# Kernel tuning notes

Measured on AMD Instinct MI355X. Metric: run time of the kernel, lower is better.

## Reference

```python
import jax, jax.numpy as jnp
import numpy as np

B, S, D, E, H, K = 4, 4096, 256, 8, 512, 2  # batch, seq, d_model, n_experts, ffn_hidden(=2*D), top_k


def setup_inputs() -> dict:
    key = jax.random.key(0)
    ks = jax.random.split(key, 6)
    x = jax.random.normal(ks[0], (B, S, D), jnp.float32)
    Wg = jax.random.normal(ks[1], (D, E), jnp.float32) * 0.02
    bg = jnp.zeros((E,), jnp.float32)
    W1 = jax.random.normal(ks[2], (E, D, H), jnp.float32) * 0.02
    b1 = jnp.zeros((E, H), jnp.float32)
    W2 = jax.random.normal(ks[3], (E, H, D), jnp.float32) * 0.02
    b2 = jnp.zeros((E, D), jnp.float32)
    return {"x": x, "Wg": Wg, "bg": bg, "W1": W1, "b1": b1, "W2": W2, "b2": b2}


def reference(x, Wg, bg, W1, b1, W2, b2):
    Bv, Sv, Dv = x.shape
    # Gate: linear -> top_k indices. NOTE: the original computes softmax(top_k scores)
    # but never uses the probabilities in the combine, so only indices matter.
    gate_scores = x @ Wg + bg                      # [B,S,E]
    _, idx = jax.lax.top_k(gate_scores, K)          # [B,S,K] (distinct experts per token)
    # Boolean membership mask per expert (0/1), matching (expert_indices == i).any(-1)
    mask = jax.nn.one_hot(idx, E, dtype=x.dtype).sum(axis=-2)  # [B,S,E]

    xf = x.reshape(-1, Dv)                          # [T,D]
    mf = mask.reshape(-1, E)                        # [T,E]
    # Dense all-experts FFN, masked combine (faithful to unweighted scatter-add).
    h = jax.nn.gelu(jnp.einsum('td,edh->teh', xf, W1) + b1[None], approximate=False)  # [T,E,H]
    y = jnp.einsum('teh,ehd->ted', h, W2) + b2[None]                                   # [T,E,D]
    out = jnp.einsum('ted,te->td', y, mf)                                              # [T,D]
    return out.reshape(Bv, Sv, Dv)
```

## Files before the change

kernel.cpp:

```cpp
#include <hip/hip_runtime.h>
#include <hip/hip_bf16.h>

#define T_TOK 16384
#define DM 256
#define NE 8
#define HF 512
#define TM 32
#define XS_LD 264

typedef __bf16 bf16x8 __attribute__((ext_vector_type(8)));
typedef float f32x4 __attribute__((ext_vector_type(4)));
typedef unsigned short u16x8 __attribute__((ext_vector_type(8)));

#define MFMA16(a, b, c) __builtin_amdgcn_mfma_f32_16x16x32_bf16((a), (b), (c), 0, 0, 0)

__device__ __forceinline__ unsigned short f2bf(float f) {
  unsigned u = __float_as_uint(f);
  u += 0x7fffu + ((u >> 16) & 1u);
  return (unsigned short)(u >> 16);
}

__device__ __forceinline__ float gelu_f(float v) {
  float s = fabsf(v) * 0.70710678118654752f;
  float t = __builtin_amdgcn_rcpf(1.0f + 0.3275911f * s);
  float p = t * (0.254829592f +
            t * (-0.284496736f +
            t * (1.421413741f +
            t * (-1.453152027f + t * 1.061405429f))));
  float e = 1.0f - p * __expf(-s * s);
  e = copysignf(e, v);
  return 0.5f * v * (1.0f + e);
}

__device__ __forceinline__ void pack_body(const float* __restrict__ in,
                                          unsigned short* __restrict__ out,
                                          int K, int N, int idx) {
  int n = idx & (N - 1);
  int rest = idx / N;
  int kq = rest & ((K >> 3) - 1);
  int eidx = rest / (K >> 3);
  int k0 = kq * 8;
  const float* src = in + ((size_t)eidx * K + k0) * N + n;
  u16x8 pk;
#pragma unroll
  for (int j = 0; j < 8; j++) pk[j] = f2bf(src[(size_t)j * N]);
  size_t baseo = (size_t)eidx * K * N +
                 (size_t)((n >> 4) * (K >> 5) + (k0 >> 5)) * 512 +
                 (size_t)(((k0 >> 3) & 3) * 128 + (n & 15) * 8);
  *reinterpret_cast<u16x8*>(out + baseo) = pk;
}

__global__ __launch_bounds__(256) void prep_kernel(
    const float* __restrict__ W1, const float* __restrict__ W2,
    unsigned short* __restrict__ w1p, unsigned short* __restrict__ w2p,
    const float* __restrict__ x, unsigned short* __restrict__ x16,
    const float* __restrict__ Wg, const float* __restrict__ bg,
    int* __restrict__ cnts, int* __restrict__ list, float* __restrict__ out) {
  __shared__ float wg_s[DM * NE];
  __shared__ int hist[NE], base_s[NE], rank[NE];
  int b = blockIdx.x;
  int tid = threadIdx.x;
  if (b < 1024) {
    float4 z = make_float4(0.f, 0.f, 0.f, 0.f);
    float4* o4 = reinterpret_cast<float4*>(out) + ((size_t)b * 256 + tid) * 4;
#pragma unroll
    for (int j = 0; j < 4; j++) o4[j] = z;
    if (b < 512) pack_body(W1, w1p, DM, HF, b * 256 + tid);
    else         pack_body(W2, w2p, HF, DM, (b - 512) * 256 + tid);
    return;
  }
  int gb = b - 1024;
  {
    float4 wv0 = *reinterpret_cast<const float4*>(Wg + tid * 8);
    float4 wv1 = *reinterpret_cast<const float4*>(Wg + tid * 8 + 4);
    *reinterpret_cast<float4*>(&wg_s[tid * 8]) = wv0;
    *reinterpret_cast<float4*>(&wg_s[tid * 8 + 4]) = wv1;
  }
  if (tid < NE) { hist[tid] = 0; rank[tid] = 0; }
  __syncthreads();

  int tl = tid >> 2;
  int cg = tid & 3;
  int t = gb * 64 + tl;
  const float* xr = x + (size_t)t * DM + cg * 64;
  unsigned short* x16r = x16 + (size_t)t * DM + cg * 64;
  double acc[NE];
#pragma unroll
  for (int i = 0; i < NE; i++) acc[i] = 0.0;
  for (int d = 0; d < 64; d += 4) {
    float4 xv = *reinterpret_cast<const float4*>(xr + d);
    {
      unsigned long long pk = (unsigned long long)f2bf(xv.x) |
                              ((unsigned long long)f2bf(xv.y) << 16) |
                              ((unsigned long long)f2bf(xv.z) << 32) |
                              ((unsigned long long)f2bf(xv.w) << 48);
      *reinterpret_cast<unsigned long long*>(x16r + d) = pk;
    }
    const float* w0 = &wg_s[(cg * 64 + d) * NE];
    float xa[4] = {xv.x, xv.y, xv.z, xv.w};
#pragma unroll
    for (int dd = 0; dd < 4; dd++) {
      float4 wa = *reinterpret_cast<const float4*>(w0 + dd * NE);
      float4 wb = *reinterpret_cast<const float4*>(w0 + dd * NE + 4);
      double xd = (double)xa[dd];
      acc[0] += xd * (double)wa.x; acc[1] += xd * (double)wa.y;
      acc[2] += xd * (double)wa.z; acc[3] += xd * (double)wa.w;
      acc[4] += xd * (double)wb.x; acc[5] += xd * (double)wb.y;
      acc[6] += xd * (double)wb.z; acc[7] += xd * (double)wb.w;
    }
  }
#pragma unroll
  for (int i = 0; i < NE; i++) {
    acc[i] += __shfl_xor(acc[i], 1, 64);
    acc[i] += __shfl_xor(acc[i], 2, 64);
    acc[i] += (double)bg[i];
  }
  int e1 = 0;
#pragma unroll
  for (int i = 1; i < NE; i++) if (acc[i] > acc[e1]) e1 = i;
  int e2 = -1;
#pragma unroll
  for (int i = 0; i < NE; i++) {
    if (i == e1) continue;
    if (e2 < 0 || acc[i] > acc[e2]) e2 = i;
  }
  if (cg == 0) {
    atomicAdd(&hist[e1], 1);
    atomicAdd(&hist[e2], 1);
  }
  __syncthreads();
  if (tid < NE) base_s[tid] = atomicAdd(&cnts[tid], hist[tid]);
  __syncthreads();
  if (cg == 0) {
    int r1 = atomicAdd(&rank[e1], 1);
    list[e1 * T_TOK + base_s[e1] + r1] = t;
    int r2 = atomicAdd(&rank[e2], 1);
    list[e2 * T_TOK + base_s[e2] + r2] = t;
  }
}

__global__ __launch_bounds__(256, 4) void ffn_kernel(
    const unsigned short* __restrict__ x16, const unsigned short* __restrict__ w1p,
    const float* __restrict__ b1, const unsigned short* __restrict__ w2p,
    const float* __restrict__ b2, const int* __restrict__ cnts,
    const int* __restrict__ list, float* __restrict__ out) {
  __shared__ unsigned short Xs[TM * XS_LD];
  __shared__ unsigned short Hl[TM * XS_LD];
  __shared__ int tok[TM];

  int e = blockIdx.x & 7;
  int tile = blockIdx.x >> 3;
  int cnt = cnts[e];
  int base = tile * TM;
  if (base >= cnt) return;
  int rowsv = min(TM, cnt - base);

  int tid = threadIdx.x;
  int w = tid >> 6, lane = tid & 63;
  int quad = lane >> 4, l16 = lane & 15;

  const unsigned short* w1e = w1p + (size_t)e * (HF * DM) + lane * 8;
  const unsigned short* w2e = w2p + (size_t)e * (DM * HF) + lane * 8;

  bf16x8 bcur[4];
#pragma unroll
  for (int nt = 0; nt < 4; nt++)
    bcur[nt] = *reinterpret_cast<const bf16x8*>(w1e + (size_t)((w * 4 + nt) * 8) * 512);

  {
    int r = tid >> 3, cg = tid & 7;
    int token = -1;
    if (r < rowsv) token = list[e * T_TOK + base + r];
    if (cg == 0) tok[r] = token;
    unsigned short* xrow = &Xs[r * XS_LD + cg * 32];
    if (token >= 0) {
      const u16x8* src = reinterpret_cast<const u16x8*>(x16 + (size_t)token * DM + cg * 32);
#pragma unroll
      for (int j = 0; j < 4; j++)
        *reinterpret_cast<u16x8*>(xrow + j * 8) = src[j];
    } else {
      u16x8 z = {0, 0, 0, 0, 0, 0, 0, 0};
#pragma unroll
      for (int j = 0; j < 4; j++)
        *reinterpret_cast<u16x8*>(xrow + j * 8) = z;
    }
  }
  __syncthreads();

  f32x4 zero4 = {0.f, 0.f, 0.f, 0.f};
  f32x4 pacc[2][4];

#pragma unroll
  for (int mt = 0; mt < 2; mt++)
#pragma unroll
    for (int nt = 0; nt < 4; nt++) pacc[mt][nt] = zero4;
#pragma unroll
  for (int ks = 0; ks < 8; ks++) {
    bf16x8 bn[4];
#pragma unroll
    for (int nt = 0; nt < 4; nt++) {
      int tn = (ks < 7) ? (w * 4 + nt) : (16 + w * 4 + nt);
      int kk = (ks < 7) ? (ks + 1) : 0;
      bn[nt] = *reinterpret_cast<const bf16x8*>(w1e + (size_t)(tn * 8 + kk) * 512);
    }
    bf16x8 a[2];
#pragma unroll
    for (int mt = 0; mt < 2; mt++)
      a[mt] = *reinterpret_cast<const bf16x8*>(&Xs[(mt * 16 + l16) * XS_LD + ks * 32 + quad * 8]);
#pragma unroll
    for (int nt = 0; nt < 4; nt++)
#pragma unroll
      for (int mt = 0; mt < 2; mt++)
        pacc[mt][nt] = MFMA16(a[mt], bcur[nt], pacc[mt][nt]);
#pragma unroll
    for (int nt = 0; nt < 4; nt++) bcur[nt] = bn[nt];
  }
#pragma unroll
  for (int nt = 0; nt < 4; nt++) {
    float bias1 = b1[e * HF + w * 64 + nt * 16 + l16];
#pragma unroll
    for (int mt = 0; mt < 2; mt++)
#pragma unroll
      for (int r = 0; r < 4; r++) {
        int row = mt * 16 + quad * 4 + r;
        Hl[row * XS_LD + w * 64 + nt * 16 + l16] = f2bf(gelu_f(pacc[mt][nt][r] + bias1));
      }
  }

#pragma unroll
  for (int mt = 0; mt < 2; mt++)
#pragma unroll
    for (int nt = 0; nt < 4; nt++) pacc[mt][nt] = zero4;
#pragma unroll
  for (int ks = 0; ks < 8; ks++) {
    bf16x8 bn[4];
#pragma unroll
    for (int nt = 0; nt < 4; nt++) {
      if (ks < 7) {
        bn[nt] = *reinterpret_cast<const bf16x8*>(
            w1e + (size_t)((16 + w * 4 + nt) * 8 + ks + 1) * 512);
      } else {
        bn[nt] = *reinterpret_cast<const bf16x8*>(w2e + (size_t)((w * 4 + nt) * 16) * 512);
      }
    }
    bf16x8 a[2];
#pragma unroll
    for (int mt = 0; mt < 2; mt++)
      a[mt] = *reinterpret_cast<const bf16x8*>(&Xs[(mt * 16 + l16) * XS_LD + ks * 32 + quad * 8]);
#pragma unroll
    for (int nt = 0; nt < 4; nt++)
#pragma unroll
      for (int mt = 0; mt < 2; mt++)
        pacc[mt][nt] = MFMA16(a[mt], bcur[nt], pacc[mt][nt]);
#pragma unroll
    for (int nt = 0; nt < 4; nt++) bcur[nt] = bn[nt];
  }
  __syncthreads();
#pragma unroll
  for (int nt = 0; nt < 4; nt++) {
    float bias1 = b1[e * HF + 256 + w * 64 + nt * 16 + l16];
#pragma unroll
    for (int mt = 0; mt < 2; mt++)
#pragma unroll
      for (int r = 0; r < 4; r++) {
        int row = mt * 16 + quad * 4 + r;
        Xs[row * XS_LD + w * 64 + nt * 16 + l16] = f2bf(gelu_f(pacc[mt][nt][r] + bias1));
      }
  }
  __syncthreads();

  f32x4 oacc[2][4];
#pragma unroll
  for (int mt = 0; mt < 2; mt++)
#pragma unroll
    for (int nt = 0; nt < 4; nt++) oacc[mt][nt] = zero4;
#pragma unroll
  for (int ks2 = 0; ks2 < 16; ks2++) {
    bf16x8 bn[4];
    if (ks2 < 15) {
#pragma unroll
      for (int nt = 0; nt < 4; nt++)
        bn[nt] = *reinterpret_cast<const bf16x8*>(
            w2e + (size_t)((w * 4 + nt) * 16 + ks2 + 1) * 512);
    }
    const unsigned short* hbase = (ks2 < 8) ? Hl : Xs;
    int col = (ks2 & 7) * 32 + quad * 8;
    bf16x8 a[2];
#pragma unroll
    for (int mt = 0; mt < 2; mt++)
      a[mt] = *reinterpret_cast<const bf16x8*>(&hbase[(mt * 16 + l16) * XS_LD + col]);
#pragma unroll
    for (int nt = 0; nt < 4; nt++)
#pragma unroll
      for (int mt = 0; mt < 2; mt++)
        oacc[mt][nt] = MFMA16(a[mt], bcur[nt], oacc[mt][nt]);
    if (ks2 < 15) {
#pragma unroll
      for (int nt = 0; nt < 4; nt++) bcur[nt] = bn[nt];
    }
  }

  float b2v[4];
#pragma unroll
  for (int nt = 0; nt < 4; nt++) b2v[nt] = b2[e * DM + w * 64 + nt * 16 + l16];
#pragma unroll
  for (int mt = 0; mt < 2; mt++) {
#pragma unroll
    for (int r = 0; r < 4; r++) {
      int m = mt * 16 + quad * 4 + r;
      int token = tok[m];
      if (token < 0) continue;
      float* orow = out + (size_t)token * DM;
#pragma unroll
      for (int nt = 0; nt < 4; nt++) {
        int d = w * 64 + nt * 16 + l16;
        atomicAdd(&orow[d], oacc[mt][nt][r] + b2v[nt]);
      }
    }
  }
}

extern "C" void kernel_launch(void* const* d_in, const int* in_sizes, int n_in,
                              void* d_out, int out_size, void* d_ws, size_t ws_size,
                              hipStream_t stream) {
  (void)in_sizes; (void)n_in; (void)ws_size; (void)out_size;
  const float* x  = (const float*)d_in[0];
  const float* Wg = (const float*)d_in[1];
  const float* bg = (const float*)d_in[2];
  const float* W1 = (const float*)d_in[3];
  const float* b1 = (const float*)d_in[4];
  const float* W2 = (const float*)d_in[5];
  const float* b2 = (const float*)d_in[6];
  float* out = (float*)d_out;

  char* ws = (char*)d_ws;
  int* cnts = (int*)ws;
  int* list = (int*)(ws + 256);
  unsigned short* w1p = (unsigned short*)(ws + 256 + 524288);
  unsigned short* w2p = (unsigned short*)(ws + 256 + 524288 + 2097152);
  unsigned short* x16 = (unsigned short*)(ws + 256 + 524288 + 2097152 + 2097152);

  hipMemsetAsync(cnts, 0, 256, stream);

  hipLaunchKernelGGL(prep_kernel, dim3(1280), dim3(256), 0, stream,
                     W1, W2, w1p, w2p, x, x16, Wg, bg, cnts, list, out);
  hipLaunchKernelGGL(ffn_kernel, dim3(NE * 512), dim3(256), 0, stream,
                     x16, w1p, b1, w2p, b2, cnts, list, out);
}
```

Before: 153.7 us.

## Use 512-thread FFN blocks with full-width hidden LDS buffer

The FFN kernel now runs 8 waves per block instead of 4. The first GEMM computes all 512 hidden columns in one pass into a single 32x520 LDS buffer, and each wave in the second GEMM covers 32 output columns instead of 64. The software-prefetch double buffering of weight fragments is removed, so fewer registers are needed per wave and more waves can hide latency. Zeroing of the output moves from prep_kernel into a hipMemsetAsync. The trade-off is a larger LDS footprint per block and no explicit prefetch of weight loads.

After: 167.6 us. 9.1% more time.

```diff
diff --git a/kernel.cpp b/kernel.cpp
--- a/kernel.cpp
+++ b/kernel.cpp
@@ -7,6 +7,7 @@
 #define HF 512
 #define TM 32
 #define XS_LD 264
+#define HC_LD 520
 
 typedef __bf16 bf16x8 __attribute__((ext_vector_type(8)));
 typedef float f32x4 __attribute__((ext_vector_type(4)));
@@ -55,18 +56,17 @@
     unsigned short* __restrict__ w1p, unsigned short* __restrict__ w2p,
     const float* __restrict__ x, unsigned short* __restrict__ x16,
     const float* __restrict__ Wg, const float* __restrict__ bg,
-    int* __restrict__ cnts, int* __restrict__ list, float* __restrict__ out) {
+    int* __restrict__ cnts, int* __restrict__ list) {
   __shared__ float wg_s[DM * NE];
   __shared__ int hist[NE], base_s[NE], rank[NE];
   int b = blockIdx.x;
   int tid = threadIdx.x;
+  if (b < 512) {
+    pack_body(W1, w1p, DM, HF, b * 256 + tid);
+    return;
+  }
   if (b < 1024) {
-    float4 z = make_float4(0.f, 0.f, 0.f, 0.f);
-    float4* o4 = reinterpret_cast<float4*>(out) + ((size_t)b * 256 + tid) * 4;
-#pragma unroll
-    for (int j = 0; j < 4; j++) o4[j] = z;
-    if (b < 512) pack_body(W1, w1p, DM, HF, b * 256 + tid);
-    else         pack_body(W2, w2p, HF, DM, (b - 512) * 256 + tid);
+    pack_body(W2, w2p, HF, DM, (b - 512) * 256 + tid);
     return;
   }
   int gb = b - 1024;
@@ -139,13 +139,13 @@
   }
 }
 
-__global__ __launch_bounds__(256, 4) void ffn_kernel(
+__global__ __launch_bounds__(512, 6) void ffn_kernel(
     const unsigned short* __restrict__ x16, const unsigned short* __restrict__ w1p,
     const float* __restrict__ b1, const unsigned short* __restrict__ w2p,
     const float* __restrict__ b2, const int* __restrict__ cnts,
     const int* __restrict__ list, float* __restrict__ out) {
   __shared__ unsigned short Xs[TM * XS_LD];
-  __shared__ unsigned short Hl[TM * XS_LD];
+  __shared__ unsigned short Hc[TM * HC_LD];
   __shared__ int tok[TM];
 
   int e = blockIdx.x & 7;
@@ -162,147 +162,87 @@
   const unsigned short* w1e = w1p + (size_t)e * (HF * DM) + lane * 8;
   const unsigned short* w2e = w2p + (size_t)e * (DM * HF) + lane * 8;
 
-  bf16x8 bcur[4];
-#pragma unroll
-  for (int nt = 0; nt < 4; nt++)
-    bcur[nt] = *reinterpret_cast<const bf16x8*>(w1e + (size_t)((w * 4 + nt) * 8) * 512);
-
   {
-    int r = tid >> 3, cg = tid & 7;
+    int r = tid >> 4, cg = tid & 15;
     int token = -1;
     if (r < rowsv) token = list[e * T_TOK + base + r];
     if (cg == 0) tok[r] = token;
-    unsigned short* xrow = &Xs[r * XS_LD + cg * 32];
+    unsigned short* xrow = &Xs[r * XS_LD + cg * 16];
     if (token >= 0) {
-      const u16x8* src = reinterpret_cast<const u16x8*>(x16 + (size_t)token * DM + cg * 32);
-#pragma unroll
-      for (int j = 0; j < 4; j++)
-        *reinterpret_cast<u16x8*>(xrow + j * 8) = src[j];
+      const u16x8* src = reinterpret_cast<const u16x8*>(x16 + (size_t)token * DM + cg * 16);
+      *reinterpret_cast<u16x8*>(xrow) = src[0];
+      *reinterpret_cast<u16x8*>(xrow + 8) = src[1];
     } else {
       u16x8 z = {0, 0, 0, 0, 0, 0, 0, 0};
-#pragma unroll
-      for (int j = 0; j < 4; j++)
-        *reinterpret_cast<u16x8*>(xrow + j * 8) = z;
+      *reinterpret_cast<u16x8*>(xrow) = z;
+      *reinterpret_cast<u16x8*>(xrow + 8) = z;
     }
   }
   __syncthreads();
 
   f32x4 zero4 = {0.f, 0.f, 0.f, 0.f};
-  f32x4 pacc[2][4];
-
+
+  {
+    f32x4 pacc[2][4];
+#pragma unroll
+    for (int mt = 0; mt < 2; mt++)
+#pragma unroll
+      for (int nt = 0; nt < 4; nt++) pacc[mt][nt] = zero4;
+#pragma unroll
+    for (int ks = 0; ks < 8; ks++) {
+      bf16x8 bfr[4];
+#pragma unroll
+      for (int nt = 0; nt < 4; nt++)
+        bfr[nt] = *reinterpret_cast<const bf16x8*>(w1e + (size_t)((w * 4 + nt) * 8 + ks) * 512);
+      bf16x8 a[2];
+#pragma unroll
+      for (int mt = 0; mt < 2; mt++)
+        a[mt] = *reinterpret_cast<const bf16x8*>(&Xs[(mt * 16 + l16) * XS_LD + ks * 32 + quad * 8]);
+#pragma unroll
+      for (int nt = 0; nt < 4; nt++)
+#pragma unroll
+        for (int mt = 0; mt < 2; mt++)
+          pacc[mt][nt] = MFMA16(a[mt], bfr[nt], pacc[mt][nt]);
+    }
+#pragma unroll
+    for (int nt = 0; nt < 4; nt++) {
+      float bias1 = b1[e * HF + w * 64 + nt * 16 + l16];
+#pragma unroll
+      for (int mt = 0; mt < 2; mt++)
+#pragma unroll
+        for (int r = 0; r < 4; r++) {
+          int row = mt * 16 + quad * 4 + r;
+          Hc[row * HC_LD + w * 64 + nt * 16 + l16] = f2bf(gelu_f(pacc[mt][nt][r] + bias1));
+        }
+    }
+  }
+  __syncthreads();
+
+  f32x4 oacc[2][2];
 #pragma unroll
   for (int mt = 0; mt < 2; mt++)
 #pragma unroll
-    for (int nt = 0; nt < 4; nt++) pacc[mt][nt] = zero4;
-#pragma unroll
-  for (int ks = 0; ks < 8; ks++) {
-    bf16x8 bn[4];
-#pragma unroll
-    for (int nt = 0; nt < 4; nt++) {
-      int tn = (ks < 7) ? (w * 4 + nt) : (16 + w * 4 + nt);
-      int kk = (ks < 7) ? (ks + 1) : 0;
-      bn[nt] = *reinterpret_cast<const bf16x8*>(w1e + (size_t)(tn * 8 + kk) * 512);
-    }
+    for (int nt = 0; nt < 2; nt++) oacc[mt][nt] = zero4;
+#pragma unroll
+  for (int ks2 = 0; ks2 < 16; ks2++) {
+    bf16x8 bfr[2];
+#pragma unroll
+    for (int nt = 0; nt < 2; nt++)
+      bfr[nt] = *reinterpret_cast<const bf16x8*>(w2e + (size_t)((w * 2 + nt) * 16 + ks2) * 512);
     bf16x8 a[2];
 #pragma unroll
     for (int mt = 0; mt < 2; mt++)
-      a[mt] = *reinterpret_cast<const bf16x8*>(&Xs[(mt * 16 + l16) * XS_LD + ks * 32 + quad * 8]);
-#pragma unroll
-    for (int nt = 0; nt < 4; nt++)
+      a[mt] = *reinterpret_cast<const bf16x8*>(&Hc[(mt * 16 + l16) * HC_LD + ks2 * 32 + quad * 8]);
+#pragma unroll
+    for (int nt = 0; nt < 2; nt++)
 #pragma unroll
       for (int mt = 0; mt < 2; mt++)
-        pacc[mt][nt] = MFMA16(a[mt], bcur[nt], pacc[mt][nt]);
-#pragma unroll
-    for (int nt = 0; nt < 4; nt++) bcur[nt] = bn[nt];
-  }
-#pragma unroll
-  for (int nt = 0; nt < 4; nt++) {
-    float bias1 = b1[e * HF + w * 64 + nt * 16 + l16];
-#pragma unroll
-    for (int mt = 0; mt < 2; mt++)
-#pragma unroll
-      for (int r = 0; r < 4; r++) {
-        int row = mt * 16 + quad * 4 + r;
-        Hl[row * XS_LD + w * 64 + nt * 16 + l16] = f2bf(gelu_f(pacc[mt][nt][r] + bias1));
-      }
-  }
-
-#pragma unroll
-  for (int mt = 0; mt < 2; mt++)
-#pragma unroll
-    for (int nt = 0; nt < 4; nt++) pacc[mt][nt] = zero4;
-#pragma unroll
-  for (int ks = 0; ks < 8; ks++) {
-    bf16x8 bn[4];
-#pragma unroll
-    for (int nt = 0; nt < 4; nt++) {
-      if (ks < 7) {
-        bn[nt] = *reinterpret_cast<const bf16x8*>(
-            w1e + (size_t)((16 + w * 4 + nt) * 8 + ks + 1) * 512);
-      } else {
-        bn[nt] = *reinterpret_cast<const bf16x8*>(w2e + (size_t)((w * 4 + nt) * 16) * 512);
-      }
-    }
-    bf16x8 a[2];
-#pragma unroll
-    for (int mt = 0; mt < 2; mt++)
-      a[mt] = *reinterpret_cast<const bf16x8*>(&Xs[(mt * 16 + l16) * XS_LD + ks * 32 + quad * 8]);
-#pragma unroll
-    for (int nt = 0; nt < 4; nt++)
-#pragma unroll
-      for (int mt = 0; mt < 2; mt++)
-        pacc[mt][nt] = MFMA16(a[mt], bcur[nt], pacc[mt][nt]);
-#pragma unroll
-    for (int nt = 0; nt < 4; nt++) bcur[nt] = bn[nt];
-  }
-  __syncthreads();
-#pragma unroll
-  for (int nt = 0; nt < 4; nt++) {
-    float bias1 = b1[e * HF + 256 + w * 64 + nt * 16 + l16];
-#pragma unroll
-    for (int mt = 0; mt < 2; mt++)
-#pragma unroll
-      for (int r = 0; r < 4; r++) {
-        int row = mt * 16 + quad * 4 + r;
-        Xs[row * XS_LD + w * 64 + nt * 16 + l16] = f2bf(gelu_f(pacc[mt][nt][r] + bias1));
-      }
-  }
-  __syncthreads();
-
-  f32x4 oacc[2][4];
-#pragma unroll
-  for (int mt = 0; mt < 2; mt++)
-#pragma unroll
-    for (int nt = 0; nt < 4; nt++) oacc[mt][nt] = zero4;
-#pragma unroll
-  for (int ks2 = 0; ks2 < 16; ks2++) {
-    bf16x8 bn[4];
-    if (ks2 < 15) {
-#pragma unroll
-      for (int nt = 0; nt < 4; nt++)
-        bn[nt] = *reinterpret_cast<const bf16x8*>(
-            w2e + (size_t)((w * 4 + nt) * 16 + ks2 + 1) * 512);
-    }
-    const unsigned short* hbase = (ks2 < 8) ? Hl : Xs;
-    int col = (ks2 & 7) * 32 + quad * 8;
-    bf16x8 a[2];
-#pragma unroll
-    for (int mt = 0; mt < 2; mt++)
-      a[mt] = *reinterpret_cast<const bf16x8*>(&hbase[(mt * 16 + l16) * XS_LD + col]);
-#pragma unroll
-    for (int nt = 0; nt < 4; nt++)
-#pragma unroll
-      for (int mt = 0; mt < 2; mt++)
-        oacc[mt][nt] = MFMA16(a[mt], bcur[nt], oacc[mt][nt]);
-    if (ks2 < 15) {
-#pragma unroll
-      for (int nt = 0; nt < 4; nt++) bcur[nt] = bn[nt];
-    }
-  }
-
-  float b2v[4];
-#pragma unroll
-  for (int nt = 0; nt < 4; nt++) b2v[nt] = b2[e * DM + w * 64 + nt * 16 + l16];
+        oacc[mt][nt] = MFMA16(a[mt], bfr[nt], oacc[mt][nt]);
+  }
+
+  float b2v[2];
+#pragma unroll
+  for (int nt = 0; nt < 2; nt++) b2v[nt] = b2[e * DM + w * 32 + nt * 16 + l16];
 #pragma unroll
   for (int mt = 0; mt < 2; mt++) {
 #pragma unroll
@@ -312,8 +252,8 @@
       if (token < 0) continue;
       float* orow = out + (size_t)token * DM;
 #pragma unroll
-      for (int nt = 0; nt < 4; nt++) {
-        int d = w * 64 + nt * 16 + l16;
+      for (int nt = 0; nt < 2; nt++) {
+        int d = w * 32 + nt * 16 + l16;
         atomicAdd(&orow[d], oacc[mt][nt][r] + b2v[nt]);
       }
     }
@@ -323,7 +263,7 @@
 extern "C" void kernel_launch(void* const* d_in, const int* in_sizes, int n_in,
                               void* d_out, int out_size, void* d_ws, size_t ws_size,
                               hipStream_t stream) {
-  (void)in_sizes; (void)n_in; (void)ws_size; (void)out_size;
+  (void)in_sizes; (void)n_in; (void)ws_size;
   const float* x  = (const float*)d_in[0];
   const float* Wg = (const float*)d_in[1];
   const float* bg = (const float*)d_in[2];
@@ -341,9 +281,10 @@
   unsigned short* x16 = (unsigned short*)(ws + 256 + 524288 + 2097152 + 2097152);
 
   hipMemsetAsync(cnts, 0, 256, stream);
+  hipMemsetAsync(d_out, 0, (size_t)out_size * sizeof(float), stream);
 
   hipLaunchKernelGGL(prep_kernel, dim3(1280), dim3(256), 0, stream,
-                     W1, W2, w1p, w2p, x, x16, Wg, bg, cnts, list, out);
-  hipLaunchKernelGGL(ffn_kernel, dim3(NE * 512), dim3(256), 0, stream,
+                     W1, W2, w1p, w2p, x, x16, Wg, bg, cnts, list);
+  hipLaunchKernelGGL(ffn_kernel, dim3(NE * 512), dim3(512), 0, stream,
                      x16, w1p, b1, w2p, b2, cnts, list, out);
 }
```
